# Optimization experiments

Measured on AMD Instinct MI355X. Metric: run time of the kernel, lower is better.

Reference implementation:

```python
import jax, jax.numpy as jnp
import numpy as np

N_NODES = 100000
N_EDGES = 3200000
F_IN, HIDDEN, N_CLASSES = 512, 256, 40


def setup_inputs() -> dict:
    key = jax.random.key(0)
    ks = jax.random.split(key, 8)
    x = jax.random.normal(ks[0], (N_NODES, F_IN), dtype=jnp.float32)
    edge_row = jax.random.randint(ks[1], (N_EDGES,), 0, N_NODES, dtype=jnp.int64)
    edge_col = jax.random.randint(ks[2], (N_EDGES,), 0, N_NODES, dtype=jnp.int64)
    edge_val = jax.random.uniform(ks[3], (N_EDGES,), dtype=jnp.float32)
    # Xavier-uniform-ish weights
    lim1 = float(np.sqrt(6.0 / (F_IN + HIDDEN)))
    lim2 = float(np.sqrt(6.0 / (HIDDEN + N_CLASSES)))
    W1 = jax.random.uniform(ks[4], (F_IN, HIDDEN), minval=-lim1, maxval=lim1, dtype=jnp.float32)
    b1 = jnp.zeros((HIDDEN,), dtype=jnp.float32)
    W2 = jax.random.uniform(ks[5], (HIDDEN, N_CLASSES), minval=-lim2, maxval=lim2, dtype=jnp.float32)
    b2 = jnp.zeros((N_CLASSES,), dtype=jnp.float32)
    return {"x": x, "edge_row": edge_row, "edge_col": edge_col, "edge_val": edge_val,
            "W1": W1, "b1": b1, "W2": W2, "b2": b2}


def _spmm(edge_row, edge_col, edge_val, h):
    # out[r] = sum_e val[e] * h[col[e]] for edges with row[e]==r  (a @ h)
    msg = edge_val[:, None] * h[edge_col]            # [E, F] gather + scale
    return jax.ops.segment_sum(msg, edge_row, num_segments=N_NODES)


def reference(x, edge_row, edge_col, edge_val, W1, b1, W2, b2):
    # Layer 1: dense mm -> spmm -> bias -> relu (dropout in eval mode = identity)
    h = _spmm(edge_row, edge_col, edge_val, x @ W1) + b1
    h = jax.nn.relu(h)
    # Layer 2: dense mm -> spmm -> bias
    logits = _spmm(edge_row, edge_col, edge_val, h @ W2) + b2
    return jax.nn.log_softmax(logits, axis=1)
```

## Files before the change

kernel.cpp:

```cpp
#include <hip/hip_runtime.h>
#include <math.h>

#define NN  100000
#define NE  3200000
#define FIN 512
#define HID 256
#define NC  40

#define NBUK 391
#define SPB  9472
#define BIN_BLOCKS 512
#define CHUNK ((NE + BIN_BLOCKS - 1) / BIN_BLOCKS)
#define COLMASK 0x1FFFF

typedef __attribute__((ext_vector_type(8))) short short8;
typedef __attribute__((ext_vector_type(4))) float f32x4;

__device__ inline float bf2f(unsigned short u) {
    unsigned int x = ((unsigned int)u) << 16;
    return __builtin_bit_cast(float, x);
}
__device__ inline unsigned short f2bfu(float f) {
    unsigned int x = __builtin_bit_cast(unsigned int, f);
    unsigned int r = (x + 0x7fffu + ((x >> 16) & 1u)) >> 16;
    return (unsigned short)r;
}
__device__ inline signed char q8(float v, float s) {
    int q = (int)rintf(v * s);
    q = max(-127, min(127, q));
    return (signed char)q;
}

__global__ __launch_bounds__(256) void k_bin(const int* __restrict__ er, const int* __restrict__ ec,
                                             const float* __restrict__ ev, int* __restrict__ bcnt,
                                             int2* __restrict__ spack) {
    __shared__ int hist[NBUK];
    __shared__ int base[NBUK];
    __shared__ int lcur[NBUK];
    for (int i = threadIdx.x; i < NBUK; i += 256) { hist[i] = 0; lcur[i] = 0; }
    __syncthreads();
    int start = blockIdx.x * CHUNK;
    int end = min(start + CHUNK, NE);
    for (int e = start + threadIdx.x; e < end; e += 256)
        atomicAdd(&hist[er[e] >> 8], 1);
    __syncthreads();
    for (int i = threadIdx.x; i < NBUK; i += 256) {
        int h = hist[i];
        base[i] = h ? atomicAdd(&bcnt[i], h) : 0;
    }
    __syncthreads();
    for (int e = start + threadIdx.x; e < end; e += 256) {
        int r = er[e];
        int b = r >> 8;
        int ofs = atomicAdd(&lcur[b], 1);
        int2 p;
        p.x = ((r & 255) << 17) | ec[e];
        p.y = __builtin_bit_cast(int, ev[e]);
        spack[(size_t)b * SPB + base[b] + ofs] = p;
    }
}

__global__ __launch_bounds__(256) void k_finecsr(const int2* __restrict__ spack, const int* __restrict__ bcnt,
                                                 int2* __restrict__ cpack,
                                                 int* __restrict__ row_beg, int* __restrict__ row_cnt) {
    __shared__ int cnt[256];
    __shared__ int sm[256];
    __shared__ int cur[256];
    int tid = threadIdx.x;
    int buk = blockIdx.x;
    size_t bb = (size_t)buk * SPB;
    int n = min(bcnt[buk], SPB);
    cnt[tid] = 0;
    __syncthreads();
    for (int i = tid; i < n; i += 256) {
        int lr = ((unsigned)spack[bb + i].x) >> 17;
        atomicAdd(&cnt[lr], 1);
    }
    __syncthreads();
    int v = cnt[tid];
    sm[tid] = v;
    __syncthreads();
    for (int off = 1; off < 256; off <<= 1) {
        int t = (tid >= off) ? sm[tid - off] : 0;
        __syncthreads();
        sm[tid] += t;
        __syncthreads();
    }
    int ex = sm[tid] - v;
    cur[tid] = ex;
    int grow = buk * 256 + tid;
    if (grow < NN) {
        row_beg[grow] = (int)bb + ex;
        row_cnt[grow] = v;
    }
    __syncthreads();
    for (int i = tid; i < n; i += 256) {
        int2 p = spack[bb + i];
        int lr = ((unsigned)p.x) >> 17;
        int pos = atomicAdd(&cur[lr], 1);
        int2 q;
        q.x = p.x & COLMASK;
        q.y = p.y;
        cpack[bb + pos] = q;
    }
}

__global__ __launch_bounds__(256) void k_w1t(const float* __restrict__ W1, unsigned short* __restrict__ W1T) {
    int b = blockIdx.x;
    int n = threadIdx.x;
    unsigned short tmp[16];
#pragma unroll
    for (int kk = 0; kk < 16; kk++)
        tmp[kk] = f2bfu(W1[(size_t)(b * 16 + kk) * HID + n]);
    unsigned short* dst = W1T + (size_t)n * FIN + b * 16;
    *(short8*)dst = *(short8*)tmp;
    *(short8*)(dst + 8) = *(short8*)(tmp + 8);
}

__global__ __launch_bounds__(256, 3) void k_gemm1(const float* __restrict__ x, const unsigned short* __restrict__ W1T,
                                                  signed char* __restrict__ h1) {
    __shared__ unsigned short As[64][40];
    __shared__ unsigned short Bs[256][40];
    const int tid = threadIdx.x;
    const int row0 = blockIdx.x * 64;
    const int lane = tid & 63;
    const int w = tid >> 6;
    const int wr = (w >> 1) * 32;
    const int wc = (w & 1) * 128;
    const int m16 = lane & 15;
    const int quad = lane >> 4;

    f32x4 acc[2][8];
#pragma unroll
    for (int i = 0; i < 2; i++)
#pragma unroll
        for (int j = 0; j < 8; j++) acc[i][j] = (f32x4){0.f, 0.f, 0.f, 0.f};

    for (int k0 = 0; k0 < FIN; k0 += 32) {
        __syncthreads();
#pragma unroll
        for (int rep = 0; rep < 2; rep++) {
            int i = tid + rep * 256;
            int r = i >> 3;
            int ks = (i & 7) * 4;
            int gr = row0 + r;
            if (gr >= NN) gr = NN - 1;
            const float4 v = *(const float4*)(x + (size_t)gr * FIN + k0 + ks);
            ushort4 b;
            b.x = f2bfu(v.x); b.y = f2bfu(v.y); b.z = f2bfu(v.z); b.w = f2bfu(v.w);
            *(ushort4*)(&As[r][ks]) = b;
        }
        {
            const unsigned short* wp = W1T + (size_t)tid * FIN + k0;
#pragma unroll
            for (int j = 0; j < 4; j++)
                *(short8*)(&Bs[tid][j * 8]) = *(const short8*)(wp + j * 8);
        }
        __syncthreads();
        short8 af[2], bfr[8];
#pragma unroll
        for (int i = 0; i < 2; i++) af[i] = *(const short8*)(&As[wr + i * 16 + m16][quad * 8]);
#pragma unroll
        for (int j = 0; j < 8; j++) bfr[j] = *(const short8*)(&Bs[wc + j * 16 + m16][quad * 8]);
#pragma unroll
        for (int i = 0; i < 2; i++)
#pragma unroll
            for (int j = 0; j < 8; j++)
                acc[i][j] = __builtin_amdgcn_mfma_f32_16x16x32_bf16(af[i], bfr[j], acc[i][j], 0, 0, 0);
    }
#pragma unroll
    for (int i = 0; i < 2; i++) {
#pragma unroll
        for (int r = 0; r < 4; r++) {
            int gr = row0 + wr + i * 16 + quad * 4 + r;
            if (gr < NN) {
#pragma unroll
                for (int j = 0; j < 8; j++) {
                    int c = wc + j * 16 + m16;
                    h1[(size_t)gr * HID + c] = q8(acc[i][j][r], 16.f);
                }
            }
        }
    }
}

__global__ __launch_bounds__(256) void k_spmm1(const signed char* __restrict__ h1,
                                               const int2* __restrict__ cpack,
                                               const int* __restrict__ row_beg, const int* __restrict__ row_cnt,
                                               const float* __restrict__ b1, unsigned short* __restrict__ a1) {
    const int lane = threadIdx.x & 63;
    const int q = lane >> 4;
    const int t = lane & 15;
    const int row = ((int)(blockIdx.x * 256 + threadIdx.x) >> 6) * 4 + q;
    if (row >= NN) return;
    const int beg = row_beg[row];
    const int end = beg + row_cnt[row];
    float s[16];
#pragma unroll
    for (int i = 0; i < 16; i++) s[i] = 0.f;
    const signed char* hp = h1 + t * 16;
    int e = beg;
    for (; e + 8 <= end; e += 8) {
        unsigned long long m[8];
#pragma unroll
        for (int j = 0; j < 8; j++)
            m[j] = __builtin_nontemporal_load((const unsigned long long*)(cpack + e + j));
        int4 g[8];
#pragma unroll
        for (int j = 0; j < 8; j++) {
            unsigned c = (unsigned)m[j];
            g[j] = *(const int4*)(hp + (size_t)(c << 8));
        }
#pragma unroll
        for (int j = 0; j < 8; j++) {
            const float v = __builtin_bit_cast(float, (unsigned)(m[j] >> 32)) * 0.0625f;
#pragma unroll
            for (int d = 0; d < 4; d++) {
                const int r = ((const int*)&g[j])[d];
                s[d * 4 + 0] = fmaf(v, (float)((r << 24) >> 24), s[d * 4 + 0]);
                s[d * 4 + 1] = fmaf(v, (float)((r << 16) >> 24), s[d * 4 + 1]);
                s[d * 4 + 2] = fmaf(v, (float)((r << 8) >> 24), s[d * 4 + 2]);
                s[d * 4 + 3] = fmaf(v, (float)(r >> 24), s[d * 4 + 3]);
            }
        }
    }
    for (; e < end; e++) {
        int2 mm = cpack[e];
        const float v = __builtin_bit_cast(float, mm.y) * 0.0625f;
        int4 gg = *(const int4*)(hp + ((size_t)(unsigned)mm.x << 8));
#pragma unroll
        for (int d = 0; d < 4; d++) {
            const int r = ((const int*)&gg)[d];
            s[d * 4 + 0] = fmaf(v, (float)((r << 24) >> 24), s[d * 4 + 0]);
            s[d * 4 + 1] = fmaf(v, (float)((r << 16) >> 24), s[d * 4 + 1]);
            s[d * 4 + 2] = fmaf(v, (float)((r << 8) >> 24), s[d * 4 + 2]);
            s[d * 4 + 3] = fmaf(v, (float)(r >> 24), s[d * 4 + 3]);
        }
    }
    const int col = t * 16;
    unsigned short o[16];
#pragma unroll
    for (int d = 0; d < 4; d++) {
        const float4 bb = *(const float4*)(b1 + col + d * 4);
        o[d * 4 + 0] = f2bfu(fmaxf(s[d * 4 + 0] + bb.x, 0.f));
        o[d * 4 + 1] = f2bfu(fmaxf(s[d * 4 + 1] + bb.y, 0.f));
        o[d * 4 + 2] = f2bfu(fmaxf(s[d * 4 + 2] + bb.z, 0.f));
        o[d * 4 + 3] = f2bfu(fmaxf(s[d * 4 + 3] + bb.w, 0.f));
    }
    unsigned short* op = a1 + (size_t)row * HID + col;
    *(short8*)op = *(short8*)o;
    *(short8*)(op + 8) = *(short8*)(o + 8);
}

__global__ __launch_bounds__(256) void k_gemm2(const unsigned short* __restrict__ a1,
                                               const float* __restrict__ W2, signed char* __restrict__ h2) {
    __shared__ float ws[HID * NC];
    for (int i = threadIdx.x; i < HID * NC; i += 256) ws[i] = W2[i];
    __syncthreads();
    int r = blockIdx.x * 32 + (threadIdx.x >> 3);
    int c0 = (threadIdx.x & 7) * 5;
    float acc[5] = {0.f, 0.f, 0.f, 0.f, 0.f};
    const unsigned short* ap = a1 + (size_t)r * HID;
    for (int k4 = 0; k4 < HID / 4; k4++) {
        ushort4 av = *(const ushort4*)(ap + k4 * 4);
        float a0 = bf2f(av.x), a1f = bf2f(av.y), a2 = bf2f(av.z), a3 = bf2f(av.w);
        const float* wp = ws + (k4 * 4) * NC + c0;
#pragma unroll
        for (int j = 0; j < 5; j++)
            acc[j] = fmaf(a0, wp[j],
                     fmaf(a1f, wp[NC + j],
                     fmaf(a2, wp[2 * NC + j],
                     fmaf(a3, wp[3 * NC + j], acc[j]))));
    }
    signed char* op = h2 + (size_t)r * 64 + c0;
#pragma unroll
    for (int j = 0; j < 5; j++) op[j] = q8(acc[j], 4.f);
}

__global__ __launch_bounds__(256) void k_spmm2(const signed char* __restrict__ h2,
                                               const int2* __restrict__ cpack,
                                               const int* __restrict__ row_beg, const int* __restrict__ row_cnt,
                                               const float* __restrict__ b2, float* __restrict__ out) {
    const int lane = threadIdx.x & 63;
    const int q = lane >> 4;
    const int t = lane & 15;
    const int row = ((int)(blockIdx.x * 256 + threadIdx.x) >> 6) * 4 + q;
    if (row >= NN) return;
    const bool act = t < 10;
    const int off = t * 4;
    const int boff = act ? off : 0;
    const int beg = row_beg[row];
    const int end = beg + row_cnt[row];
    float a[4] = {0.f, 0.f, 0.f, 0.f};
    const signed char* hp = h2 + off;
    int e = beg;
    for (; e + 8 <= end; e += 8) {
        unsigned long long m[8];
#pragma unroll
        for (int j = 0; j < 8; j++)
            m[j] = __builtin_nontemporal_load((const unsigned long long*)(cpack + e + j));
        int g[8];
#pragma unroll
        for (int j = 0; j < 8; j++) {
            unsigned c = (unsigned)m[j];
            g[j] = *(const int*)(hp + (size_t)(c << 6));
        }
#pragma unroll
        for (int j = 0; j < 8; j++) {
            const float v = __builtin_bit_cast(float, (unsigned)(m[j] >> 32)) * 0.25f;
            const int r = g[j];
            a[0] = fmaf(v, (float)((r << 24) >> 24), a[0]);
            a[1] = fmaf(v, (float)((r << 16) >> 24), a[1]);
            a[2] = fmaf(v, (float)((r << 8) >> 24), a[2]);
            a[3] = fmaf(v, (float)(r >> 24), a[3]);
        }
    }
    for (; e < end; e++) {
        int2 mm = cpack[e];
        const float v = __builtin_bit_cast(float, mm.y) * 0.25f;
        const int r = *(const int*)(hp + ((size_t)(unsigned)mm.x << 6));
        a[0] = fmaf(v, (float)((r << 24) >> 24), a[0]);
        a[1] = fmaf(v, (float)((r << 16) >> 24), a[1]);
        a[2] = fmaf(v, (float)((r << 8) >> 24), a[2]);
        a[3] = fmaf(v, (float)(r >> 24), a[3]);
    }
    const float4 bb = *(const float4*)(b2 + boff);
    float acc[4];
    acc[0] = a[0] + bb.x; acc[1] = a[1] + bb.y; acc[2] = a[2] + bb.z; acc[3] = a[3] + bb.w;
    float mx = act ? fmaxf(fmaxf(acc[0], acc[1]), fmaxf(acc[2], acc[3])) : -INFINITY;
#pragma unroll
    for (int o = 1; o < 16; o <<= 1) mx = fmaxf(mx, __shfl_xor(mx, o, 16));
    float se = 0.f;
    if (act) {
#pragma unroll
        for (int i = 0; i < 4; i++) se += expf(acc[i] - mx);
    }
#pragma unroll
    for (int o = 1; o < 16; o <<= 1) se += __shfl_xor(se, o, 16);
    const float ls = logf(se);
    if (act) {
        float4 r;
        r.x = acc[0] - mx - ls;
        r.y = acc[1] - mx - ls;
        r.z = acc[2] - mx - ls;
        r.w = acc[3] - mx - ls;
        *(float4*)(out + (size_t)row * NC + off) = r;
    }
}

extern "C" void kernel_launch(void* const* d_in, const int* in_sizes, int n_in, void* d_out, int out_size,
                              void* d_ws, size_t ws_size, hipStream_t stream) {
    const float* x  = (const float*)d_in[0];
    const int*   er = (const int*)d_in[1];
    const int*   ec = (const int*)d_in[2];
    const float* ev = (const float*)d_in[3];
    const float* W1 = (const float*)d_in[4];
    const float* b1 = (const float*)d_in[5];
    const float* W2 = (const float*)d_in[6];
    const float* b2 = (const float*)d_in[7];
    float* out = (float*)d_out;
    char* ws = (char*)d_ws;

    int2*  spack       = (int2*)(ws + 0);
    signed char* h1    = (signed char*)(ws + 0);
    unsigned short* a1 = (unsigned short*)(ws + 29628416);
    signed char* h2    = (signed char*)(ws + 80828416);
    int2*  cpack       = (int2*)(ws + 87228416);
    int*   row_beg     = (int*)(ws + 116856832);
    int*   row_cnt     = (int*)(ws + 117256832);
    int*   bcnt        = (int*)(ws + 117656832);
    unsigned short* W1T = (unsigned short*)(ws + 117658880);

    hipMemsetAsync(bcnt, 0, NBUK * sizeof(int), stream);
    k_w1t<<<32, 256, 0, stream>>>(W1, W1T);
    k_bin<<<BIN_BLOCKS, 256, 0, stream>>>(er, ec, ev, bcnt, spack);
    k_finecsr<<<NBUK, 256, 0, stream>>>(spack, bcnt, cpack, row_beg, row_cnt);
    k_gemm1<<<(NN + 63) / 64, 256, 0, stream>>>(x, W1T, h1);
    k_spmm1<<<(NN + 15) / 16, 256, 0, stream>>>(h1, cpack, row_beg, row_cnt, b1, a1);
    k_gemm2<<<NN / 32, 256, 0, stream>>>(a1, W2, h2);
    k_spmm2<<<(NN + 15) / 16, 256, 0, stream>>>(h2, cpack, row_beg, row_cnt, b2, out);
}
```

Baseline: 731.3 us.

## Double-buffer gemm1 with 128x128 tiles and move gemm2 to bf16 MFMA

gemm1 now uses 128x128 output tiles split across two column blocks, with a double-buffered LDS pipeline that prefetches the next K slice into registers while the current one is computed. It also converts to bf16 with the packed hardware convert instruction. gemm2 is rewritten from a scalar FP32 shared-memory loop to bf16 MFMA, reading a pre-transposed, zero-padded W2T that a new small kernel produces. The aim is to cut GEMM time, at the cost of x being re-read twice in gemm1 and W2 being rounded to bf16.

```diff
diff --git a/kernel.cpp b/kernel.cpp
--- a/kernel.cpp
+++ b/kernel.cpp
@@ -29,6 +29,11 @@
     int q = (int)rintf(v * s);
     q = max(-127, min(127, q));
     return (signed char)q;
+}
+__device__ inline unsigned cvtpk_bf16(float lo, float hi) {
+    unsigned r;
+    asm("v_cvt_pk_bf16_f32 %0, %1, %2" : "=v"(r) : "v"(lo), "v"(hi));
+    return r;
 }
 
 __global__ __launch_bounds__(256) void k_bin(const int* __restrict__ er, const int* __restrict__ ec,
@@ -117,66 +122,107 @@
     *(short8*)(dst + 8) = *(short8*)(tmp + 8);
 }
 
-__global__ __launch_bounds__(256, 3) void k_gemm1(const float* __restrict__ x, const unsigned short* __restrict__ W1T,
-                                                  signed char* __restrict__ h1) {
-    __shared__ unsigned short As[64][40];
-    __shared__ unsigned short Bs[256][40];
+__global__ __launch_bounds__(256) void k_w2t(const float* __restrict__ W2, unsigned short* __restrict__ W2T) {
+    int n = blockIdx.x;
+    int k = threadIdx.x;
+    float v = (n < NC) ? W2[(size_t)k * NC + n] : 0.f;
+    W2T[(size_t)n * HID + k] = f2bfu(v);
+}
+
+__global__ __launch_bounds__(256) void k_gemm1(const float* __restrict__ x, const unsigned short* __restrict__ W1T,
+                                               signed char* __restrict__ h1) {
+    __shared__ unsigned short As[2][128][40];
+    __shared__ unsigned short Bs[2][128][40];
     const int tid = threadIdx.x;
-    const int row0 = blockIdx.x * 64;
+    const int row0 = (blockIdx.x >> 1) * 128;
+    const int col0 = (blockIdx.x & 1) * 128;
     const int lane = tid & 63;
     const int w = tid >> 6;
-    const int wr = (w >> 1) * 32;
-    const int wc = (w & 1) * 128;
+    const int wr = (w >> 1) * 64;
+    const int wc = (w & 1) * 64;
     const int m16 = lane & 15;
     const int quad = lane >> 4;
 
-    f32x4 acc[2][8];
-#pragma unroll
-    for (int i = 0; i < 2; i++)
-#pragma unroll
-        for (int j = 0; j < 8; j++) acc[i][j] = (f32x4){0.f, 0.f, 0.f, 0.f};
-
-    for (int k0 = 0; k0 < FIN; k0 += 32) {
+    const int srow = tid >> 1;
+    const int skoff = (tid & 1) * 16;
+    int gar = row0 + srow;
+    if (gar >= NN) gar = NN - 1;
+    const float* ax = x + (size_t)gar * FIN + skoff;
+    const unsigned short* bw = W1T + (size_t)(col0 + srow) * FIN + skoff;
+
+    f32x4 acc[4][4];
+#pragma unroll
+    for (int i = 0; i < 4; i++)
+#pragma unroll
+        for (int j = 0; j < 4; j++) acc[i][j] = (f32x4){0.f, 0.f, 0.f, 0.f};
+
+    float4 va[4];
+    uint4 vb0, vb1;
+
+#define G1_LOAD(tt)                                                        \
+    {                                                                      \
+        const float* ap = ax + (tt) * 32;                                  \
+        va[0] = *(const float4*)(ap);                                      \
+        va[1] = *(const float4*)(ap + 4);                                  \
+        va[2] = *(const float4*)(ap + 8);                                  \
+        va[3] = *(const float4*)(ap + 12);                                 \
+        const unsigned short* bp = bw + (tt) * 32;                         \
+        vb0 = *(const uint4*)(bp);                                         \
+        vb1 = *(const uint4*)(bp + 8);                                     \
+    }
+
+#define G1_STORE(bf)                                                       \
+    {                                                                      \
+        uint4 pa0, pa1;                                                    \
+        pa0.x = cvtpk_bf16(va[0].x, va[0].y);                              \
+        pa0.y = cvtpk_bf16(va[0].z, va[0].w);                              \
+        pa0.z = cvtpk_bf16(va[1].x, va[1].y);                              \
+        pa0.w = cvtpk_bf16(va[1].z, va[1].w);                              \
+        pa1.x = cvtpk_bf16(va[2].x, va[2].y);                              \
+        pa1.y = cvtpk_bf16(va[2].z, va[2].w);                              \
+        pa1.z = cvtpk_bf16(va[3].x, va[3].y);                              \
+        pa1.w = cvtpk_bf16(va[3].z, va[3].w);                              \
+        *(uint4*)(&As[bf][srow][skoff]) = pa0;                             \
+        *(uint4*)(&As[bf][srow][skoff + 8]) = pa1;                         \
+        *(uint4*)(&Bs[bf][srow][skoff]) = vb0;                             \
+        *(uint4*)(&Bs[bf][srow][skoff + 8]) = vb1;                         \
+    }
+
+    G1_LOAD(0)
+    G1_STORE(0)
+    G1_LOAD(1)
+    __syncthreads();
+
+    for (int t = 0; t < 16; ++t) {
+        const int buf = t & 1;
+        short8 af[4], bfr[4];
+#pragma unroll
+        for (int i = 0; i < 4; i++) af[i] = *(const short8*)(&As[buf][wr + i * 16 + m16][quad * 8]);
+#pragma unroll
+        for (int j = 0; j < 4; j++) bfr[j] = *(const short8*)(&Bs[buf][wc + j * 16 + m16][quad * 8]);
+        if (t < 15) {
+            G1_STORE(buf ^ 1)
+            if (t < 14) G1_LOAD(t + 2)
+        }
+#pragma unroll
+        for (int i = 0; i < 4; i++)
+#pragma unroll
+            for (int j = 0; j < 4; j++)
+                acc[i][j] = __builtin_amdgcn_mfma_f32_16x16x32_bf16(af[i], bfr[j], acc[i][j], 0, 0, 0);
         __syncthreads();
-#pragma unroll
-        for (int rep = 0; rep < 2; rep++) {
-            int i = tid + rep * 256;
-            int r = i >> 3;
-            int ks = (i & 7) * 4;
-            int gr = row0 + r;
-            if (gr >= NN) gr = NN - 1;
-            const float4 v = *(const float4*)(x + (size_t)gr * FIN + k0 + ks);
-            ushort4 b;
-            b.x = f2bfu(v.x); b.y = f2bfu(v.y); b.z = f2bfu(v.z); b.w = f2bfu(v.w);
-            *(ushort4*)(&As[r][ks]) = b;
-        }
-        {
-            const unsigned short* wp = W1T + (size_t)tid * FIN + k0;
-#pragma unroll
-            for (int j = 0; j < 4; j++)
-                *(short8*)(&Bs[tid][j * 8]) = *(const short8*)(wp + j * 8);
-        }
-        __syncthreads();
-        short8 af[2], bfr[8];
-#pragma unroll
-        for (int i = 0; i < 2; i++) af[i] = *(const short8*)(&As[wr + i * 16 + m16][quad * 8]);
-#pragma unroll
-        for (int j = 0; j < 8; j++) bfr[j] = *(const short8*)(&Bs[wc + j * 16 + m16][quad * 8]);
-#pragma unroll
-        for (int i = 0; i < 2; i++)
-#pragma unroll
-            for (int j = 0; j < 8; j++)
-                acc[i][j] = __builtin_amdgcn_mfma_f32_16x16x32_bf16(af[i], bfr[j], acc[i][j], 0, 0, 0);
-    }
-#pragma unroll
-    for (int i = 0; i < 2; i++) {
+    }
+#undef G1_LOAD
+#undef G1_STORE
+
+#pragma unroll
+    for (int i = 0; i < 4; i++) {
 #pragma unroll
         for (int r = 0; r < 4; r++) {
             int gr = row0 + wr + i * 16 + quad * 4 + r;
             if (gr < NN) {
 #pragma unroll
-                for (int j = 0; j < 8; j++) {
-                    int c = wc + j * 16 + m16;
+                for (int j = 0; j < 4; j++) {
+                    int c = col0 + wc + j * 16 + m16;
                     h1[(size_t)gr * HID + c] = q8(acc[i][j][r], 16.f);
                 }
             }
@@ -253,28 +299,51 @@
 }
 
 __global__ __launch_bounds__(256) void k_gemm2(const unsigned short* __restrict__ a1,
-                                               const float* __restrict__ W2, signed char* __restrict__ h2) {
-    __shared__ float ws[HID * NC];
-    for (int i = threadIdx.x; i < HID * NC; i += 256) ws[i] = W2[i];
-    __syncthreads();
-    int r = blockIdx.x * 32 + (threadIdx.x >> 3);
-    int c0 = (threadIdx.x & 7) * 5;
-    float acc[5] = {0.f, 0.f, 0.f, 0.f, 0.f};
-    const unsigned short* ap = a1 + (size_t)r * HID;
-    for (int k4 = 0; k4 < HID / 4; k4++) {
-        ushort4 av = *(const ushort4*)(ap + k4 * 4);
-        float a0 = bf2f(av.x), a1f = bf2f(av.y), a2 = bf2f(av.z), a3 = bf2f(av.w);
-        const float* wp = ws + (k4 * 4) * NC + c0;
-#pragma unroll
-        for (int j = 0; j < 5; j++)
-            acc[j] = fmaf(a0, wp[j],
-                     fmaf(a1f, wp[NC + j],
-                     fmaf(a2, wp[2 * NC + j],
-                     fmaf(a3, wp[3 * NC + j], acc[j]))));
-    }
-    signed char* op = h2 + (size_t)r * 64 + c0;
-#pragma unroll
-    for (int j = 0; j < 5; j++) op[j] = q8(acc[j], 4.f);
+                                               const unsigned short* __restrict__ W2T, signed char* __restrict__ h2) {
+    const int tid = threadIdx.x;
+    const int lane = tid & 63;
+    const int w = tid >> 6;
+    const int m16 = lane & 15;
+    const int quad = lane >> 4;
+    const int r0 = blockIdx.x * 256 + w * 64;
+
+    f32x4 acc[4][3];
+#pragma unroll
+    for (int i = 0; i < 4; i++)
+#pragma unroll
+        for (int j = 0; j < 3; j++) acc[i][j] = (f32x4){0.f, 0.f, 0.f, 0.f};
+
+    for (int k0 = 0; k0 < HID; k0 += 32) {
+        short8 af[4], bfr[3];
+#pragma unroll
+        for (int i = 0; i < 4; i++) {
+            int gr = r0 + i * 16 + m16;
+            if (gr >= NN) gr = NN - 1;
+            af[i] = *(const short8*)(a1 + (size_t)gr * HID + k0 + quad * 8);
+        }
+#pragma unroll
+        for (int j = 0; j < 3; j++)
+            bfr[j] = *(const short8*)(W2T + (size_t)(j * 16 + m16) * HID + k0 + quad * 8);
+#pragma unroll
+        for (int i = 0; i < 4; i++)
+#pragma unroll
+            for (int j = 0; j < 3; j++)
+                acc[i][j] = __builtin_amdgcn_mfma_f32_16x16x32_bf16(af[i], bfr[j], acc[i][j], 0, 0, 0);
+    }
+#pragma unroll
+    for (int i = 0; i < 4; i++) {
+#pragma unroll
+        for (int r = 0; r < 4; r++) {
+            int gr = r0 + i * 16 + quad * 4 + r;
+            if (gr < NN) {
+#pragma unroll
+                for (int j = 0; j < 3; j++) {
+                    int c = j * 16 + m16;
+                    if (c < NC) h2[(size_t)gr * 64 + c] = q8(acc[i][j][r], 4.f);
+                }
+            }
+        }
+    }
 }
 
 __global__ __launch_bounds__(256) void k_spmm2(const signed char* __restrict__ h2,
@@ -370,13 +439,15 @@
     int*   row_cnt     = (int*)(ws + 117256832);
     int*   bcnt        = (int*)(ws + 117656832);
     unsigned short* W1T = (unsigned short*)(ws + 117658880);
+    unsigned short* W2T = (unsigned short*)(ws + 117921024);
 
     hipMemsetAsync(bcnt, 0, NBUK * sizeof(int), stream);
     k_w1t<<<32, 256, 0, stream>>>(W1, W1T);
+    k_w2t<<<48, 256, 0, stream>>>(W2, W2T);
     k_bin<<<BIN_BLOCKS, 256, 0, stream>>>(er, ec, ev, bcnt, spack);
     k_finecsr<<<NBUK, 256, 0, stream>>>(spack, bcnt, cpack, row_beg, row_cnt);
-    k_gemm1<<<(NN + 63) / 64, 256, 0, stream>>>(x, W1T, h1);
+    k_gemm1<<<1564, 256, 0, stream>>>(x, W1T, h1);
     k_spmm1<<<(NN + 15) / 16, 256, 0, stream>>>(h1, cpack, row_beg, row_cnt, b1, a1);
-    k_gemm2<<<NN / 32, 256, 0, stream>>>(a1, W2, h2);
+    k_gemm2<<<(NN + 255) / 256, 256, 0, stream>>>(a1, W2T, h2);
     k_spmm2<<<(NN + 15) / 16, 256, 0, stream>>>(h2, cpack, row_beg, row_cnt, b2, out);
 }
```

After: 654.8 us. 10.5% less time.
